# Kernel tuning notes

Hardware: AMD Instinct MI355X
Metric: run time of the kernel (lower is better)

Reference implementation:

```python
import jax, jax.numpy as jnp
import numpy as np


def _causal_kernel_mask(K):
    # casual_mask[i, K-i:] = 0 for i in 1..p
    p = K // 2
    m = np.ones((p + 1, K), np.float32)
    for i in range(1, p + 1):
        m[i, K - i:] = 0.0
    return jnp.asarray(m)


def setup_inputs() -> dict:
    rng = jax.random.key(0)
    k0, k1, k2, k3, k4 = jax.random.split(rng, 5)
    B, H, N, F = 2, 16, 1024, 64
    V, K = 32000, 5
    return {
        "input_ids": jax.random.randint(k0, (B, N), 0, V),
        "query": jax.random.normal(k1, (B, H, N, F), dtype=jnp.float32),
        "key": jax.random.normal(k2, (B, H, N, F), dtype=jnp.float32),
        "value": jax.random.normal(k3, (B, H, N, F), dtype=jnp.float32),
        "emb_weight": jax.random.normal(k4, (V, 2 * K), dtype=jnp.float32) * 0.02,
    }


def reference(input_ids, query, key, value, emb_weight):
    B, H, N, F = query.shape
    K = emb_weight.shape[1] // 2  # head/layer invariant -> emb dim = 2*K
    p = K // 2
    G = 2 * H

    # ---- get_kernel (layer 0; head_invariant + layer_invariant) ----
    kern = emb_weight[input_ids]                       # [B,N,2K]
    kern = kern.reshape(B, N, 2, 1, K)                 # [B,N,2,1,K]
    kern = jnp.broadcast_to(kern, (B, N, 2, H, K)).reshape(B, N, G, K)

    # ---- conv_key_value (for_casual=True, strict_on_casual=True) ----
    kv = jnp.concatenate([key, value], axis=1)         # [B,2H,N,F]
    kv_pad = jnp.pad(kv, ((0, 0), (0, 0), (p, p), (0, 0)))
    # unfold over token dim: [B,2H,K,N,F]
    kv_unf = jnp.stack([kv_pad[:, :, k:k + N, :] for k in range(K)], axis=2)
    cmask = _causal_kernel_mask(K)                     # [p+1,K]
    kern_m = kern[:, :, :, None, :] * cmask[None, None, None]  # [B,N,2H,p+1,K]
    # dynamic depthwise conv with per-offset causal masking
    out = jnp.einsum('bgknf,bngjk->bgjnf', kv_unf, kern_m)     # [B,2H,p+1,N,F]
    key_c = out[:, :H, 0]                              # [B,H,N,F]
    value_c = out[:, H:, 0]                            # [B,H,N,F]

    # ---- attention with causal-boundary corrections (n_past = 0) ----
    scale = 1.0 / jnp.sqrt(jnp.asarray(F, dtype=query.dtype))
    q = query * scale
    scores = jnp.einsum('bhnf,bhmf->bhnm', q, key_c)   # [B,H,N,N]

    # correct_attn_weights_near_casual_boundary
    for i in range(p):
        off = p - 1 - i
        cb_key = out[:, :H, 1 + i]                     # [B,H,N,F]
        corr = jnp.einsum('bhnf,bhnf->bhn', q[:, :, off:, :], cb_key[:, :, :N - off, :])
        rows = jnp.arange(N - off) + off
        cols = jnp.arange(N - off)
        scores = scores.at[:, :, rows, cols].set(corr)

    causal = jnp.tril(jnp.ones((N, N), dtype=bool))
    scores = jnp.where(causal, scores, jnp.asarray(-1e9, dtype=scores.dtype))
    probs = jax.nn.softmax(scores, axis=-1)
    attn = jnp.einsum('bhnm,bhmf->bhnf', probs, value_c)

    # correct_attn_output_near_casual_boundary
    for i in range(p):
        off = p - 1 - i
        cb_value = out[:, H:, 1 + i]                   # [B,H,N,F]
        idx = jnp.arange(N - off)
        diag_w = probs[:, :, idx + off, idx]           # diag offset=-off: [B,H,N-off]
        diff_v = cb_value[:, :, :N - off, :] - value_c[:, :, :N - off, :]
        diff = diag_w[..., None] * diff_v
        attn = attn + jnp.pad(diff, ((0, 0), (0, 0), (off, 0), (0, 0)))

    return attn
```

## Files before the change

kernel.cpp:

```cpp
#include <hip/hip_runtime.h>

#define HD    64
#define NSEQ  1024
#define NPB   12
#define LOG2E 1.44269504088896f

typedef __attribute__((ext_vector_type(8))) __bf16 bf16x8;
typedef __attribute__((ext_vector_type(4))) float  f32x4;
typedef __attribute__((ext_vector_type(4))) unsigned short u16x4;

__device__ __constant__ unsigned char PAIRS12[NPB] = {
    6, 8, 10, 12, 14, 15, 4, 13, 2, 11, 0, 9 };

__device__ inline unsigned short f2bf(float x) {
    unsigned u = __float_as_uint(x);
    return (unsigned short)((u + 0x7fffu + ((u >> 16) & 1u)) >> 16);
}
__device__ inline unsigned pk2(float a, float b) {
    return (unsigned)f2bf(a) | ((unsigned)f2bf(b) << 16);
}
__device__ inline float dot4(f32x4 a, f32x4 b) {
    return a.x * b.x + a.y * b.y + a.z * b.z + a.w * b.w;
}

__global__ __launch_bounds__(256) void conv_kernel(
    const int* __restrict__ ids,
    const float* __restrict__ keyg,
    const float* __restrict__ valg,
    const float* __restrict__ qg,
    const float* __restrict__ emb,
    unsigned short* __restrict__ kc,
    unsigned short* __restrict__ vcT,
    float* __restrict__ dg1, float* __restrict__ dg2)
{
    __shared__ __align__(16) float sA[70 * 68];
    __shared__ __align__(16) float sB[70 * 68];
    __shared__ float sE[65 * 10];

    int pid = blockIdx.x;
    int bh = pid & 31;
    int n0 = (pid >> 5) << 6;
    int b  = bh >> 4;
    int t  = threadIdx.x;
    size_t hb = (size_t)bh * NSEQ * HD;
    const float* kb = keyg + hb;
    const float* vb = valg + hb;

    for (int u = t; u < 650; u += 256) {
        int r = u / 10, c = u - r * 10;
        int n = n0 - 1 + r;
        sE[u] = (n >= 0) ? emb[(size_t)ids[b * NSEQ + n] * 10 + c] : 0.f;
    }
    for (int u = t; u < 70 * 16; u += 256) {
        int r = u >> 4, f = (u & 15) << 2;
        int g = n0 - 3 + r;
        f32x4 kv4 = (f32x4){0.f, 0.f, 0.f, 0.f};
        f32x4 vv4 = (f32x4){0.f, 0.f, 0.f, 0.f};
        if (g >= 0 && g < NSEQ) {
            kv4 = *(const f32x4*)(kb + (size_t)g * HD + f);
            vv4 = *(const f32x4*)(vb + (size_t)g * HD + f);
        }
        *(f32x4*)(sA + r * 68 + f) = kv4;
        *(f32x4*)(sB + r * 68 + f) = vv4;
    }
    __syncthreads();

    f32x4 vcv_save[4];
#pragma unroll
    for (int i = 0; i < 4; ++i) {
        int u  = (i << 8) + t;
        int nl = u >> 4, g4 = u & 15;
        int n  = n0 + nl, f = g4 << 2;
        const float* e  = sE + (nl + 1) * 10;
        const float* ep = sE + nl * 10;
        const float* ar = sA + nl * 68 + f;
        const float* br = sB + nl * 68 + f;
        f32x4 km3 = *(const f32x4*)(ar);
        f32x4 x0 = *(const f32x4*)(ar + 68);
        f32x4 x1 = *(const f32x4*)(ar + 2 * 68);
        f32x4 x2 = *(const f32x4*)(ar + 3 * 68);
        f32x4 x3 = *(const f32x4*)(ar + 4 * 68);
        f32x4 x4 = *(const f32x4*)(ar + 5 * 68);
        f32x4 v0 = *(const f32x4*)(br + 68);
        f32x4 v1 = *(const f32x4*)(br + 2 * 68);
        f32x4 v2 = *(const f32x4*)(br + 3 * 68);
        f32x4 v3 = *(const f32x4*)(br + 4 * 68);
        f32x4 v4 = *(const f32x4*)(br + 5 * 68);
        f32x4 qv = *(const f32x4*)(qg + hb + (size_t)n * HD + f) * (0.125f * LOG2E);

        f32x4 k012 = e[0] * x0 + e[1] * x1 + e[2] * x2;
        f32x4 kcv  = k012 + e[3] * x3 + e[4] * x4;
        f32x4 vcv  = e[5] * v0 + e[6] * v1 + e[7] * v2 + e[8] * v3 + e[9] * v4;

        u16x4 kq;
        kq.x = f2bf(kcv.x); kq.y = f2bf(kcv.y); kq.z = f2bf(kcv.z); kq.w = f2bf(kcv.w);
        *(u16x4*)(kc + hb + (size_t)n * HD + f) = kq;
        vcv_save[i] = vcv;

        float s2 = dot4(qv, k012);
        f32x4 kj1 = ep[0] * km3 + ep[1] * x0 + ep[2] * x1 + ep[3] * x2;
        float s1 = dot4(qv, kj1);
#pragma unroll
        for (int o = 1; o < 16; o <<= 1) {
            s2 += __shfl_xor(s2, o, 64);
            s1 += __shfl_xor(s1, o, 64);
        }
        if (g4 == 0) {
            dg2[bh * NSEQ + n] = s2;
            dg1[bh * NSEQ + n] = s1;
        }
    }
    __syncthreads();
    float* vt = sA;
#pragma unroll
    for (int i = 0; i < 4; ++i) {
        int u = (i << 8) + t;
        int nl = u >> 4, f = (u & 15) << 2;
        *(f32x4*)(vt + nl * 68 + f) = vcv_save[i];
    }
    __syncthreads();
#pragma unroll
    for (int i = 0; i < 4; ++i) {
        int u = (i << 8) + t;
        int f = u >> 4, nn = (u & 15) << 2;
        u16x4 o;
        o.x = f2bf(vt[(nn + 0) * 68 + f]);
        o.y = f2bf(vt[(nn + 1) * 68 + f]);
        o.z = f2bf(vt[(nn + 2) * 68 + f]);
        o.w = f2bf(vt[(nn + 3) * 68 + f]);
        *(u16x4*)(vcT + ((size_t)bh * HD + f) * NSEQ + n0 + nn) = o;
    }
}

__global__ __launch_bounds__(512, 4) void attn_kernel(
    const float* __restrict__ qg,
    const unsigned short* __restrict__ kc,
    const unsigned short* __restrict__ vcT,
    const float* __restrict__ dg1, const float* __restrict__ dg2,
    const float* __restrict__ valg, const int* __restrict__ ids,
    const float* __restrict__ emb,
    float* __restrict__ pML, unsigned short* __restrict__ pO,
    float* __restrict__ outg)
{
    __shared__ __align__(16) unsigned char sK[2][8192];
    __shared__ __align__(16) unsigned char sV[2][8192];
    __shared__ __align__(16) unsigned char sP[16384];

    int pid  = blockIdx.x;
    int bh   = pid & 31;
    int slot = pid >> 5;
    int code = PAIRS12[slot];
    int jj = code >> 1, cch = code & 1;
    int t0 = cch << 3;
    int ntile = 2 * jj + 2;
    int len = cch ? (ntile - 8) : (ntile > 8 ? 8 : ntile);

    int t = threadIdx.x;
    int wv = t >> 6, l = t & 63;
    int w_in = wv & 3;
    int my_j = 2 * jj + (wv >> 2);
    int nc  = (my_j >= 8) ? 2 : 1;
    int lq = l & 15, h = l >> 4, l7 = l & 7;
    int lid = h * 16 + lq;
    int qbw = my_j * 64 + w_in * 16;
    size_t hb = (size_t)bh * NSEQ * HD;

    const unsigned short* kcb = kc  + hb;
    const unsigned short* vtb = vcT + (size_t)bh * HD * NSEQ;

    bf16x8 qb0, qb1;
    {
        const float* qr = qg + hb + (size_t)(qbw + lq) * HD + 8 * h;
        f32x4 a0 = *(const f32x4*)(qr);
        f32x4 a1 = *(const f32x4*)(qr + 4);
        f32x4 b0 = *(const f32x4*)(qr + 32);
        f32x4 b1 = *(const f32x4*)(qr + 36);
        const float S = 0.125f * LOG2E;
        union { unsigned u[4]; bf16x8 v; } u0, u1;
        u0.u[0] = pk2(a0.x * S, a0.y * S); u0.u[1] = pk2(a0.z * S, a0.w * S);
        u0.u[2] = pk2(a1.x * S, a1.y * S); u0.u[3] = pk2(a1.z * S, a1.w * S);
        u1.u[0] = pk2(b0.x * S, b0.y * S); u1.u[1] = pk2(b0.z * S, b0.w * S);
        u1.u[2] = pk2(b1.x * S, b1.y * S); u1.u[3] = pk2(b1.z * S, b1.w * S);
        qb0 = u0.v; qb1 = u1.v;
    }
    float diag2_l = dg2[bh * NSEQ + qbw + lq];
    float diag1_l = dg1[bh * NSEQ + qbw + lq];

    f32x4 of[4];
#pragma unroll
    for (int ft = 0; ft < 4; ++ft) of[ft] = (f32x4){0.f, 0.f, 0.f, 0.f};
    float m_run = -1e30f, denom = 0.f;

    const int ka_off0 = ((0 + h) ^ l7) << 4;
    const int ka_off1 = ((4 + h) ^ l7) << 4;
    const int pr_base = wv * 2048 + lq * 128;
    const int chk0 = ((qbw > 0 ? qbw - 1 : 0) >> 6);

    const int s_r0 = (t & 511) >> 3, s_c0 = t & 7;
    const int s_cs0 = s_c0 ^ (s_r0 & 7);
    const int s_buf0 = t >> 9;
    const int s_r1 = ((t + 512) & 511) >> 3, s_c1 = (t + 512) & 7;
    const int s_cs1 = s_c1 ^ (s_r1 & 7);
    const int s_buf1 = (t + 512) >> 9;

    uint4 pf[2];
    auto issue = [&](int tg) {
        int kv0 = tg << 6;
        pf[0] = (s_buf0 == 0)
            ? *(const uint4*)(kcb + (size_t)(kv0 + s_r0) * HD + s_cs0 * 8)
            : *(const uint4*)(vtb + (size_t)s_r0 * NSEQ + kv0 + s_cs0 * 8);
        pf[1] = (s_buf1 == 0)
            ? *(const uint4*)(kcb + (size_t)(kv0 + s_r1) * HD + s_cs1 * 8)
            : *(const uint4*)(vtb + (size_t)s_r1 * NSEQ + kv0 + s_cs1 * 8);
    };
    auto commit = [&](int cu) {
        *(uint4*)((s_buf0 ? sV[cu] : sK[cu]) + s_r0 * 128 + s_c0 * 16) = pf[0];
        *(uint4*)((s_buf1 ? sV[cu] : sK[cu]) + s_r1 * 128 + s_c1 * 16) = pf[1];
    };

    issue(t0); commit(0);
    if (len > 1) issue(t0 + 1);
    __syncthreads();

    for (int ti = 0; ti < len; ++ti) {
        int cur = ti & 1;
        if (ti + 1 < len) commit(cur ^ 1);
        if (ti + 2 < len) issue(t0 + ti + 2);
        int tg  = t0 + ti;
        int kv0 = tg << 6;
        bool act = (tg <= my_j);

        if (act) {
            const unsigned char* sKc = sK[cur];
            const unsigned char* sVc = sV[cur];
            f32x4 p[4];
            __builtin_amdgcn_s_setprio(1);
#pragma unroll
            for (int st = 0; st < 4; ++st) {
                bf16x8 ka0 = *(const bf16x8*)(sKc + st * 2048 + lq * 128 + ka_off0);
                bf16x8 ka1 = *(const bf16x8*)(sKc + st * 2048 + lq * 128 + ka_off1);
                f32x4 d = (f32x4){0.f, 0.f, 0.f, 0.f};
                d = __builtin_amdgcn_mfma_f32_16x16x32_bf16(ka0, qb0, d, 0, 0, 0);
                d = __builtin_amdgcn_mfma_f32_16x16x32_bf16(ka1, qb1, d, 0, 0, 0);
                p[st] = d;
            }
            __builtin_amdgcn_s_setprio(0);

            if (tg >= chk0) {
                int n_l = qbw + lq;
#pragma unroll
                for (int st = 0; st < 4; ++st)
#pragma unroll
                    for (int r = 0; r < 4; ++r) {
                        int kv = kv0 + st * 16 + 4 * h + r;
                        float dd = p[st][r];
                        if (kv > n_l)           dd = -1e30f;
                        else if (kv == n_l)     dd = diag2_l;
                        else if (kv == n_l - 1) dd = diag1_l;
                        p[st][r] = dd;
                    }
            }

            float tmax = -1e30f;
#pragma unroll
            for (int st = 0; st < 4; ++st)
#pragma unroll
                for (int r = 0; r < 4; ++r) tmax = fmaxf(tmax, p[st][r]);
            tmax = fmaxf(tmax, __shfl_xor(tmax, 16, 64));
            tmax = fmaxf(tmax, __shfl_xor(tmax, 32, 64));
            if (!__all(tmax <= m_run + 7.0f)) {
                float m_new = fmaxf(m_run, tmax);
                float alpha = __builtin_exp2f(m_run - m_new);
                denom *= alpha;
                m_run = m_new;
#pragma unroll
                for (int r = 0; r < 4; ++r) {
                    float ar = __shfl(alpha, 4 * h + r, 64);
                    of[0][r] *= ar; of[1][r] *= ar; of[2][r] *= ar; of[3][r] *= ar;
                }
            }
            float lsum = 0.f;
#pragma unroll
            for (int st = 0; st < 4; ++st)
#pragma unroll
                for (int r = 0; r < 4; ++r) {
                    float e = __builtin_exp2f(p[st][r] - m_run);
                    p[st][r] = e;
                    lsum += e;
                }
            lsum += __shfl_xor(lsum, 16, 64);
            lsum += __shfl_xor(lsum, 32, 64);
            denom += lsum;

#pragma unroll
            for (int st = 0; st < 4; ++st) {
                uint2 uu;
                uu.x = pk2(p[st][0], p[st][1]);
                uu.y = pk2(p[st][2], p[st][3]);
                int chunk = (st << 1) + (h >> 1);
                *(uint2*)(sP + pr_base + ((chunk ^ l7) << 4) + ((h & 1) << 3)) = uu;
            }
            asm volatile("s_waitcnt lgkmcnt(0)" ::: "memory");
            __builtin_amdgcn_sched_barrier(0);

            __builtin_amdgcn_s_setprio(1);
#pragma unroll
            for (int kk = 0; kk < 2; ++kk) {
                int koff = kk ? ka_off1 : ka_off0;
                bf16x8 pa = *(const bf16x8*)(sP + pr_base + koff);
#pragma unroll
                for (int ft = 0; ft < 4; ++ft) {
                    bf16x8 vb = *(const bf16x8*)(sVc + ft * 2048 + lq * 128 + koff);
                    of[ft] = __builtin_amdgcn_mfma_f32_16x16x32_bf16(pa, vb, of[ft], 0, 0, 0);
                }
            }
            __builtin_amdgcn_s_setprio(0);
        }
        if (ti + 1 < len) __syncthreads();
    }

    int psBase = ((bh << 4) | my_j) << 2;
    if (nc > 1) {
        if (h == 0) {
            float2 ml; ml.x = m_run; ml.y = denom;
            *(float2*)(pML + ((size_t)(psBase + cch) * 64 + w_in * 16 + lq) * 2) = ml;
        }
#pragma unroll
        for (int ft = 0; ft < 4; ++ft)
#pragma unroll
            for (int r = 0; r < 4; ++r)
                pO[(size_t)((((psBase + cch) * 4 + w_in) * 4 + ft) * 4 + r) * 64 + lid] =
                    f2bf(of[ft][r]);
        return;
    }

    const float* vraw = valg + hb;
    float* outr = outg + hb;
    const int* idb = ids + (size_t)(bh >> 4) * NSEQ;
#pragma unroll
    for (int r = 0; r < 4; ++r) {
        int qrow = 4 * h + r;
        int n = qbw + qrow;
        float dn = __shfl(denom,   qrow, 64);
        float mf = __shfl(m_run,   qrow, 64);
        float d2 = __shfl(diag2_l, qrow, 64);
        float d1 = __shfl(diag1_l, qrow, 64);
        float inv = 1.0f / dn;
        float p2 = __builtin_exp2f(d2 - mf) * inv;
        float p1 = (n >= 1) ? __builtin_exp2f(d1 - mf) * inv : 0.f;
        int id_n = idb[n];
        float e8  = emb[(size_t)id_n * 10 + 8];
        float e9  = emb[(size_t)id_n * 10 + 9];
        float e9p = (n >= 1) ? emb[(size_t)idb[n - 1] * 10 + 9] : 0.f;
        float ca = -(p2 * e8 + p1 * e9p);
        float cb = -p2 * e9;
#pragma unroll
        for (int ft = 0; ft < 4; ++ft) {
            int f = ft * 16 + lq;
            float v = of[ft][r] * inv;
            if (n + 1 < NSEQ) v += ca * vraw[(size_t)(n + 1) * HD + f];
            if (n + 2 < NSEQ) v += cb * vraw[(size_t)(n + 2) * HD + f];
            outr[(size_t)n * HD + f] = v;
        }
    }
}

__global__ __launch_bounds__(256) void merge_kernel(
    const float* __restrict__ pML, const unsigned short* __restrict__ pO,
    const float* __restrict__ dg1, const float* __restrict__ dg2,
    const float* __restrict__ valg, const int* __restrict__ ids,
    const float* __restrict__ emb, float* __restrict__ outg)
{
    int pid = blockIdx.x;
    int bh = pid & 31, j = (pid >> 5) + 8;
    int t = threadIdx.x;
    int rloc = t >> 2, fg = t & 3;
    int n = (j << 6) + rloc;
    int f0 = fg << 4;
    size_t hb = (size_t)bh * NSEQ * HD;
    int psBase = ((bh << 4) | j) << 2;

    float mc[2], lc[2];
#pragma unroll
    for (int c = 0; c < 2; ++c) {
        float2 v = *(const float2*)(pML + ((size_t)(psBase + c) * 64 + rloc) * 2);
        mc[c] = v.x; lc[c] = v.y;
    }
    float mg = fmaxf(mc[0], mc[1]);
    float D = 0.f;
    f32x4 a0 = (f32x4){0.f,0.f,0.f,0.f}, a1 = a0, a2 = a0, a3 = a0;
#pragma unroll
    for (int c = 0; c < 2; ++c) {
        float wc = __builtin_exp2f(mc[c] - mg);
        D += lc[c] * wc;
        const unsigned short* pp = pO +
            (size_t)((((psBase + c) * 4 + (rloc >> 4)) * 4 + fg) * 4 + (rloc & 3)) * 64
            + ((rloc >> 2) & 3) * 16;
        uint4 ua = *(const uint4*)(pp);
        uint4 ub = *(const uint4*)(pp + 8);
        a0.x += wc * __uint_as_float(ua.x << 16);
        a0.y += wc * __uint_as_float(ua.x & 0xffff0000u);
        a0.z += wc * __uint_as_float(ua.y << 16);
        a0.w += wc * __uint_as_float(ua.y & 0xffff0000u);
        a1.x += wc * __uint_as_float(ua.z << 16);
        a1.y += wc * __uint_as_float(ua.z & 0xffff0000u);
        a1.z += wc * __uint_as_float(ua.w << 16);
        a1.w += wc * __uint_as_float(ua.w & 0xffff0000u);
        a2.x += wc * __uint_as_float(ub.x << 16);
        a2.y += wc * __uint_as_float(ub.x & 0xffff0000u);
        a2.z += wc * __uint_as_float(ub.y << 16);
        a2.w += wc * __uint_as_float(ub.y & 0xffff0000u);
        a3.x += wc * __uint_as_float(ub.z << 16);
        a3.y += wc * __uint_as_float(ub.z & 0xffff0000u);
        a3.z += wc * __uint_as_float(ub.w << 16);
        a3.w += wc * __uint_as_float(ub.w & 0xffff0000u);
    }
    float inv = 1.0f / D;
    float d2 = dg2[bh * NSEQ + n], d1 = dg1[bh * NSEQ + n];
    float p2 = __builtin_exp2f(d2 - mg) * inv;
    float p1 = __builtin_exp2f(d1 - mg) * inv;
    const int* idb = ids + (size_t)(bh >> 4) * NSEQ;
    int id_n = idb[n];
    float e8  = emb[(size_t)id_n * 10 + 8];
    float e9  = emb[(size_t)id_n * 10 + 9];
    float e9p = emb[(size_t)idb[n - 1] * 10 + 9];
    float ca = -(p2 * e8 + p1 * e9p);
    float cb = -p2 * e9;

    a0 *= inv; a1 *= inv; a2 *= inv; a3 *= inv;
    if (n + 1 < NSEQ) {
        const float* v1 = valg + hb + (size_t)(n + 1) * HD + f0;
        a0 += ca * *(const f32x4*)(v1);
        a1 += ca * *(const f32x4*)(v1 + 4);
        a2 += ca * *(const f32x4*)(v1 + 8);
        a3 += ca * *(const f32x4*)(v1 + 12);
    }
    if (n + 2 < NSEQ) {
        const float* v2 = valg + hb + (size_t)(n + 2) * HD + f0;
        a0 += cb * *(const f32x4*)(v2);
        a1 += cb * *(const f32x4*)(v2 + 4);
        a2 += cb * *(const f32x4*)(v2 + 8);
        a3 += cb * *(const f32x4*)(v2 + 12);
    }
    float* o = outg + hb + (size_t)n * HD + f0;
    *(f32x4*)(o)      = a0;
    *(f32x4*)(o + 4)  = a1;
    *(f32x4*)(o + 8)  = a2;
    *(f32x4*)(o + 12) = a3;
}

extern "C" void kernel_launch(void* const* d_in, const int* in_sizes, int n_in,
                              void* d_out, int out_size, void* d_ws, size_t ws_size,
                              hipStream_t stream)
{
    const int*   ids = (const int*)  d_in[0];
    const float* q   = (const float*)d_in[1];
    const float* key = (const float*)d_in[2];
    const float* val = (const float*)d_in[3];
    const float* emb = (const float*)d_in[4];
    float* out = (float*)d_out;

    char* w = (char*)d_ws;
    unsigned short* kc  = (unsigned short*)(w);
    unsigned short* vcT = (unsigned short*)(w + (4u << 20));
    float* dg1 = (float*)(w + 8388608);
    float* dg2 = (float*)(w + 8519680);
    float* pML = (float*)(w + 8650752);
    unsigned short* pO = (unsigned short*)(w + 9699328);

    conv_kernel<<<512, 256, 0, stream>>>(ids, key, val, q, emb, kc, vcT, dg1, dg2);
    attn_kernel<<<32 * NPB, 512, 0, stream>>>(q, kc, vcT, dg1, dg2, val, ids, emb,
                                              pML, pO, out);
    merge_kernel<<<256, 256, 0, stream>>>(pML, pO, dg1, dg2, val, ids, emb, out);
}
```

Measured before the change: 50.51 us.

## Split attention into 4-tile KV chunks per query block and drop running max

Reorganizes attn_kernel from 512-thread blocks covering paired query blocks with up to 8 KV tiles into 256-thread blocks, each handling one 64-row query block against a chunk of at most 4 KV tiles. That gives 1280 blocks and up to 4 partials per query block, which merge_kernel combines. It also removes online-softmax max tracking and rescaling, exponentiating raw scores on the assumption that values stay bounded. The aim is better load balance and occupancy and less softmax work, at the cost of more partial-result traffic and overflow risk for large scores.

```diff
diff --git a/kernel.cpp b/kernel.cpp
--- a/kernel.cpp
+++ b/kernel.cpp
@@ -2,15 +2,17 @@
 
 #define HD    64
 #define NSEQ  1024
-#define NPB   12
+#define NSLOT 40
 #define LOG2E 1.44269504088896f
 
 typedef __attribute__((ext_vector_type(8))) __bf16 bf16x8;
 typedef __attribute__((ext_vector_type(4))) float  f32x4;
 typedef __attribute__((ext_vector_type(4))) unsigned short u16x4;
 
-__device__ __constant__ unsigned char PAIRS12[NPB] = {
-    6, 8, 10, 12, 14, 15, 4, 13, 2, 11, 0, 9 };
+__device__ __constant__ unsigned char PAIRS[NSLOT] = {
+    60,61,62,63, 56,57,58, 52,53,54, 48,49,50, 44,45,46,
+    40,41, 36,37, 32,33, 28,29, 24, 20, 16, 12,
+    59, 42, 25, 8, 55, 38, 21, 4, 51, 34, 17, 0 };
 
 __device__ inline unsigned short f2bf(float x) {
     unsigned u = __float_as_uint(x);
@@ -132,7 +134,7 @@
     }
 }
 
-__global__ __launch_bounds__(512, 4) void attn_kernel(
+__global__ __launch_bounds__(256, 4) void attn_kernel(
     const float* __restrict__ qg,
     const unsigned short* __restrict__ kc,
     const unsigned short* __restrict__ vcT,
@@ -144,25 +146,23 @@
 {
     __shared__ __align__(16) unsigned char sK[2][8192];
     __shared__ __align__(16) unsigned char sV[2][8192];
-    __shared__ __align__(16) unsigned char sP[16384];
+    __shared__ __align__(16) unsigned char sP[8192];
 
     int pid  = blockIdx.x;
     int bh   = pid & 31;
     int slot = pid >> 5;
-    int code = PAIRS12[slot];
-    int jj = code >> 1, cch = code & 1;
-    int t0 = cch << 3;
-    int ntile = 2 * jj + 2;
-    int len = cch ? (ntile - 8) : (ntile > 8 ? 8 : ntile);
+    int code = PAIRS[slot];
+    int j = code >> 2, cch = code & 3;
+    int q0 = j << 6;
+    int t0 = cch << 2;
+    int len = j - (cch << 2) + 1; if (len > 4) len = 4;
+    int nc  = (j >> 2) + 1;
 
     int t = threadIdx.x;
-    int wv = t >> 6, l = t & 63;
-    int w_in = wv & 3;
-    int my_j = 2 * jj + (wv >> 2);
-    int nc  = (my_j >= 8) ? 2 : 1;
+    int w = t >> 6, l = t & 63;
     int lq = l & 15, h = l >> 4, l7 = l & 7;
     int lid = h * 16 + lq;
-    int qbw = my_j * 64 + w_in * 16;
+    int qbw = q0 + w * 16;
     size_t hb = (size_t)bh * NSEQ * HD;
 
     const unsigned short* kcb = kc  + hb;
@@ -189,33 +189,35 @@
     f32x4 of[4];
 #pragma unroll
     for (int ft = 0; ft < 4; ++ft) of[ft] = (f32x4){0.f, 0.f, 0.f, 0.f};
-    float m_run = -1e30f, denom = 0.f;
+    float denom = 0.f;
 
     const int ka_off0 = ((0 + h) ^ l7) << 4;
     const int ka_off1 = ((4 + h) ^ l7) << 4;
-    const int pr_base = wv * 2048 + lq * 128;
+    const int pr_base = w * 2048 + lq * 128;
     const int chk0 = ((qbw > 0 ? qbw - 1 : 0) >> 6);
 
-    const int s_r0 = (t & 511) >> 3, s_c0 = t & 7;
-    const int s_cs0 = s_c0 ^ (s_r0 & 7);
-    const int s_buf0 = t >> 9;
-    const int s_r1 = ((t + 512) & 511) >> 3, s_c1 = (t + 512) & 7;
-    const int s_cs1 = s_c1 ^ (s_r1 & 7);
-    const int s_buf1 = (t + 512) >> 9;
-
-    uint4 pf[2];
+    uint4 pf[4];
     auto issue = [&](int tg) {
         int kv0 = tg << 6;
-        pf[0] = (s_buf0 == 0)
-            ? *(const uint4*)(kcb + (size_t)(kv0 + s_r0) * HD + s_cs0 * 8)
-            : *(const uint4*)(vtb + (size_t)s_r0 * NSEQ + kv0 + s_cs0 * 8);
-        pf[1] = (s_buf1 == 0)
-            ? *(const uint4*)(kcb + (size_t)(kv0 + s_r1) * HD + s_cs1 * 8)
-            : *(const uint4*)(vtb + (size_t)s_r1 * NSEQ + kv0 + s_cs1 * 8);
+#pragma unroll
+        for (int i = 0; i < 4; ++i) {
+            int chunk = t + (i << 8);
+            int buf = chunk >> 9, loc = chunk & 511;
+            int r = loc >> 3, c = loc & 7;
+            int cs = c ^ (r & 7);
+            pf[i] = (buf == 0)
+                ? *(const uint4*)(kcb + (size_t)(kv0 + r) * HD + cs * 8)
+                : *(const uint4*)(vtb + (size_t)r * NSEQ + kv0 + cs * 8);
+        }
     };
     auto commit = [&](int cu) {
-        *(uint4*)((s_buf0 ? sV[cu] : sK[cu]) + s_r0 * 128 + s_c0 * 16) = pf[0];
-        *(uint4*)((s_buf1 ? sV[cu] : sK[cu]) + s_r1 * 128 + s_c1 * 16) = pf[1];
+#pragma unroll
+        for (int i = 0; i < 4; ++i) {
+            int chunk = t + (i << 8);
+            int buf = chunk >> 9, loc = chunk & 511;
+            int r = loc >> 3, c = loc & 7;
+            *(uint4*)((buf ? sV[cu] : sK[cu]) + r * 128 + c * 16) = pf[i];
+        }
     };
 
     issue(t0); commit(0);
@@ -228,108 +230,87 @@
         if (ti + 2 < len) issue(t0 + ti + 2);
         int tg  = t0 + ti;
         int kv0 = tg << 6;
-        bool act = (tg <= my_j);
-
-        if (act) {
-            const unsigned char* sKc = sK[cur];
-            const unsigned char* sVc = sV[cur];
-            f32x4 p[4];
-            __builtin_amdgcn_s_setprio(1);
-#pragma unroll
-            for (int st = 0; st < 4; ++st) {
-                bf16x8 ka0 = *(const bf16x8*)(sKc + st * 2048 + lq * 128 + ka_off0);
-                bf16x8 ka1 = *(const bf16x8*)(sKc + st * 2048 + lq * 128 + ka_off1);
-                f32x4 d = (f32x4){0.f, 0.f, 0.f, 0.f};
-                d = __builtin_amdgcn_mfma_f32_16x16x32_bf16(ka0, qb0, d, 0, 0, 0);
-                d = __builtin_amdgcn_mfma_f32_16x16x32_bf16(ka1, qb1, d, 0, 0, 0);
-                p[st] = d;
+        const unsigned char* sKc = sK[cur];
+        const unsigned char* sVc = sV[cur];
+
+        f32x4 p[4];
+        __builtin_amdgcn_s_setprio(1);
+#pragma unroll
+        for (int st = 0; st < 4; ++st) {
+            bf16x8 ka0 = *(const bf16x8*)(sKc + st * 2048 + lq * 128 + ka_off0);
+            bf16x8 ka1 = *(const bf16x8*)(sKc + st * 2048 + lq * 128 + ka_off1);
+            f32x4 d = (f32x4){0.f, 0.f, 0.f, 0.f};
+            d = __builtin_amdgcn_mfma_f32_16x16x32_bf16(ka0, qb0, d, 0, 0, 0);
+            d = __builtin_amdgcn_mfma_f32_16x16x32_bf16(ka1, qb1, d, 0, 0, 0);
+            p[st] = d;
+        }
+        __builtin_amdgcn_s_setprio(0);
+
+        if (tg >= chk0) {
+            int n_l = qbw + lq;
+#pragma unroll
+            for (int st = 0; st < 4; ++st)
+#pragma unroll
+                for (int r = 0; r < 4; ++r) {
+                    int kv = kv0 + st * 16 + 4 * h + r;
+                    float dd = p[st][r];
+                    if (kv > n_l)           dd = -1e30f;
+                    else if (kv == n_l)     dd = diag2_l;
+                    else if (kv == n_l - 1) dd = diag1_l;
+                    p[st][r] = dd;
+                }
+        }
+
+        float lsum = 0.f;
+#pragma unroll
+        for (int st = 0; st < 4; ++st)
+#pragma unroll
+            for (int r = 0; r < 4; ++r) {
+                float e = __builtin_exp2f(p[st][r]);
+                p[st][r] = e;
+                lsum += e;
             }
-            __builtin_amdgcn_s_setprio(0);
-
-            if (tg >= chk0) {
-                int n_l = qbw + lq;
-#pragma unroll
-                for (int st = 0; st < 4; ++st)
-#pragma unroll
-                    for (int r = 0; r < 4; ++r) {
-                        int kv = kv0 + st * 16 + 4 * h + r;
-                        float dd = p[st][r];
-                        if (kv > n_l)           dd = -1e30f;
-                        else if (kv == n_l)     dd = diag2_l;
-                        else if (kv == n_l - 1) dd = diag1_l;
-                        p[st][r] = dd;
-                    }
+        lsum += __shfl_xor(lsum, 16, 64);
+        lsum += __shfl_xor(lsum, 32, 64);
+        denom += lsum;
+
+#pragma unroll
+        for (int st = 0; st < 4; ++st) {
+            uint2 uu;
+            uu.x = pk2(p[st][0], p[st][1]);
+            uu.y = pk2(p[st][2], p[st][3]);
+            int chunk = (st << 1) + (h >> 1);
+            *(uint2*)(sP + pr_base + ((chunk ^ l7) << 4) + ((h & 1) << 3)) = uu;
+        }
+        asm volatile("s_waitcnt lgkmcnt(0)" ::: "memory");
+        __builtin_amdgcn_sched_barrier(0);
+
+        __builtin_amdgcn_s_setprio(1);
+#pragma unroll
+        for (int kk = 0; kk < 2; ++kk) {
+            int koff = kk ? ka_off1 : ka_off0;
+            bf16x8 pa = *(const bf16x8*)(sP + pr_base + koff);
+#pragma unroll
+            for (int ft = 0; ft < 4; ++ft) {
+                bf16x8 vb = *(const bf16x8*)(sVc + ft * 2048 + lq * 128 + koff);
+                of[ft] = __builtin_amdgcn_mfma_f32_16x16x32_bf16(pa, vb, of[ft], 0, 0, 0);
             }
-
-            float tmax = -1e30f;
-#pragma unroll
-            for (int st = 0; st < 4; ++st)
-#pragma unroll
-                for (int r = 0; r < 4; ++r) tmax = fmaxf(tmax, p[st][r]);
-            tmax = fmaxf(tmax, __shfl_xor(tmax, 16, 64));
-            tmax = fmaxf(tmax, __shfl_xor(tmax, 32, 64));
-            if (!__all(tmax <= m_run + 7.0f)) {
-                float m_new = fmaxf(m_run, tmax);
-                float alpha = __builtin_exp2f(m_run - m_new);
-                denom *= alpha;
-                m_run = m_new;
-#pragma unroll
-                for (int r = 0; r < 4; ++r) {
-                    float ar = __shfl(alpha, 4 * h + r, 64);
-                    of[0][r] *= ar; of[1][r] *= ar; of[2][r] *= ar; of[3][r] *= ar;
-                }
-            }
-            float lsum = 0.f;
-#pragma unroll
-            for (int st = 0; st < 4; ++st)
-#pragma unroll
-                for (int r = 0; r < 4; ++r) {
-                    float e = __builtin_exp2f(p[st][r] - m_run);
-                    p[st][r] = e;
-                    lsum += e;
-                }
-            lsum += __shfl_xor(lsum, 16, 64);
-            lsum += __shfl_xor(lsum, 32, 64);
-            denom += lsum;
-
-#pragma unroll
-            for (int st = 0; st < 4; ++st) {
-                uint2 uu;
-                uu.x = pk2(p[st][0], p[st][1]);
-                uu.y = pk2(p[st][2], p[st][3]);
-                int chunk = (st << 1) + (h >> 1);
-                *(uint2*)(sP + pr_base + ((chunk ^ l7) << 4) + ((h & 1) << 3)) = uu;
-            }
-            asm volatile("s_waitcnt lgkmcnt(0)" ::: "memory");
-            __builtin_amdgcn_sched_barrier(0);
-
-            __builtin_amdgcn_s_setprio(1);
-#pragma unroll
-            for (int kk = 0; kk < 2; ++kk) {
-                int koff = kk ? ka_off1 : ka_off0;
-                bf16x8 pa = *(const bf16x8*)(sP + pr_base + koff);
-#pragma unroll
-                for (int ft = 0; ft < 4; ++ft) {
-                    bf16x8 vb = *(const bf16x8*)(sVc + ft * 2048 + lq * 128 + koff);
-                    of[ft] = __builtin_amdgcn_mfma_f32_16x16x32_bf16(pa, vb, of[ft], 0, 0, 0);
-                }
-            }
-            __builtin_amdgcn_s_setprio(0);
-        }
+        }
+        __builtin_amdgcn_s_setprio(0);
         if (ti + 1 < len) __syncthreads();
     }
 
-    int psBase = ((bh << 4) | my_j) << 2;
+    int psBase = ((bh << 4) | j) << 2;
     if (nc > 1) {
         if (h == 0) {
-            float2 ml; ml.x = m_run; ml.y = denom;
-            *(float2*)(pML + ((size_t)(psBase + cch) * 64 + w_in * 16 + lq) * 2) = ml;
+            float2 ml; ml.x = 0.f; ml.y = denom;
+            *(float2*)(pML + ((size_t)(psBase + cch) * 64 + w * 16 + lq) * 2) = ml;
         }
 #pragma unroll
         for (int ft = 0; ft < 4; ++ft)
 #pragma unroll
             for (int r = 0; r < 4; ++r)
-                pO[(size_t)((((psBase + cch) * 4 + w_in) * 4 + ft) * 4 + r) * 64 + lid] =
+                pO[(size_t)((((psBase + cch) * 4 + w) * 4 + ft) * 4 + r) * 64 + lid] =
                     f2bf(of[ft][r]);
         return;
     }
@@ -342,12 +323,11 @@
         int qrow = 4 * h + r;
         int n = qbw + qrow;
         float dn = __shfl(denom,   qrow, 64);
-        float mf = __shfl(m_run,   qrow, 64);
         float d2 = __shfl(diag2_l, qrow, 64);
         float d1 = __shfl(diag1_l, qrow, 64);
         float inv = 1.0f / dn;
-        float p2 = __builtin_exp2f(d2 - mf) * inv;
-        float p1 = (n >= 1) ? __builtin_exp2f(d1 - mf) * inv : 0.f;
+        float p2 = __builtin_exp2f(d2) * inv;
+        float p1 = (n >= 1) ? __builtin_exp2f(d1) * inv : 0.f;
         int id_n = idb[n];
         float e8  = emb[(size_t)id_n * 10 + 8];
         float e9  = emb[(size_t)id_n * 10 + 9];
@@ -372,7 +352,8 @@
     const float* __restrict__ emb, float* __restrict__ outg)
 {
     int pid = blockIdx.x;
-    int bh = pid & 31, j = (pid >> 5) + 8;
+    int bh = pid & 31, j = (pid >> 5) + 4;
+    int nc = (j >> 2) + 1;
     int t = threadIdx.x;
     int rloc = t >> 2, fg = t & 3;
     int n = (j << 6) + rloc;
@@ -380,17 +361,16 @@
     size_t hb = (size_t)bh * NSEQ * HD;
     int psBase = ((bh << 4) | j) << 2;
 
-    float mc[2], lc[2];
-#pragma unroll
-    for (int c = 0; c < 2; ++c) {
+    float mc[4], lc[4];
+    float mg = -3e30f;
+    for (int c = 0; c < nc; ++c) {
         float2 v = *(const float2*)(pML + ((size_t)(psBase + c) * 64 + rloc) * 2);
         mc[c] = v.x; lc[c] = v.y;
-    }
-    float mg = fmaxf(mc[0], mc[1]);
+        mg = fmaxf(mg, mc[c]);
+    }
     float D = 0.f;
     f32x4 a0 = (f32x4){0.f,0.f,0.f,0.f}, a1 = a0, a2 = a0, a3 = a0;
-#pragma unroll
-    for (int c = 0; c < 2; ++c) {
+    for (int c = 0; c < nc; ++c) {
         float wc = __builtin_exp2f(mc[c] - mg);
         D += lc[c] * wc;
         const unsigned short* pp = pO +
@@ -469,7 +449,7 @@
     unsigned short* pO = (unsigned short*)(w + 9699328);
 
     conv_kernel<<<512, 256, 0, stream>>>(ids, key, val, q, emb, kc, vcT, dg1, dg2);
-    attn_kernel<<<32 * NPB, 512, 0, stream>>>(q, kc, vcT, dg1, dg2, val, ids, emb,
-                                              pML, pO, out);
-    merge_kernel<<<256, 256, 0, stream>>>(pML, pO, dg1, dg2, val, ids, emb, out);
-}
+    attn_kernel<<<32 * NSLOT, 256, 0, stream>>>(q, kc, vcT, dg1, dg2, val, ids, emb,
+                                                pML, pO, out);
+    merge_kernel<<<384, 256, 0, stream>>>(pML, pO, dg1, dg2, val, ids, emb, out);
+}
```

After: 56.16 us. 1.11x slower.
